# Kernel optimization log

Measured on AMD Instinct MI355X. Metric: run time of the kernel, lower is better.

Reference implementation:

```python
import jax, jax.numpy as jnp
import numpy as np


def setup_inputs() -> dict:
    key = jax.random.key(0)
    k1, k2 = jax.random.split(key)
    B, N, M = 8, 8192, 8192
    pred = jax.random.normal(k1, (B, N, 3), dtype=jnp.float32)
    gt = jax.random.normal(k2, (B, M, 3), dtype=jnp.float32)
    return {"pred": pred, "gt": gt}


def _chamfer(pred, gt):
    # pred: [B,N,3], gt: [B,M,3]
    # squared pairwise distances: ||p||^2 + ||q||^2 - 2 p.q  -> [B,N,M]
    p_sq = jnp.sum(pred * pred, axis=-1)           # [B,N]
    q_sq = jnp.sum(gt * gt, axis=-1)               # [B,M]
    cross = jnp.einsum('bnd,bmd->bnm', pred, gt)   # [B,N,M]
    dist = p_sq[:, :, None] + q_sq[:, None, :] - 2.0 * cross
    dist = jnp.maximum(dist, 0.0)  # numerical floor, distances are non-negative
    # kaolin chamfer_distance: mean over points of nearest-neighbor sq-dist, both sides
    p2q = jnp.mean(jnp.min(dist, axis=2), axis=1)  # [B]
    q2p = jnp.mean(jnp.min(dist, axis=1), axis=1)  # [B]
    chamfer = p2q + q2p                            # [B] (w1 = w2 = 1)
    return jnp.mean(chamfer)                       # scalar, torch.mean over batch


def reference(pred, gt):
    return _chamfer(pred, gt)
```

## Files before the change

### kernel.cpp

```cpp
#include <hip/hip_runtime.h>


typedef short bf16x8 __attribute__((ext_vector_type(8)));
typedef float f32x16 __attribute__((ext_vector_type(16)));

#define B_SZ   8
#define NPTS   8192
#define TOTAL  (B_SZ * NPTS)
#define BLOCK  256
#define QB     256
#define SLICE  1024
#define NSTAGE (NPTS / SLICE)
#define TILES  (SLICE / 32)

__device__ __forceinline__ unsigned short bf16rn(float f, float* rem) {
    unsigned u = __float_as_uint(f);
    unsigned h = (u + 0x8000u) & 0xFFFF0000u;
    *rem = f - __uint_as_float(h);
    return (unsigned short)(h >> 16);
}

__global__ __launch_bounds__(BLOCK) void chamfer_prep_mfma(
    const float* __restrict__ gt, const float* __restrict__ pred,
    uint4* __restrict__ TgA, uint4* __restrict__ TgB, float* __restrict__ Wg,
    uint4* __restrict__ TpA, uint4* __restrict__ TpB, float* __restrict__ Wp)
{
    int i = blockIdx.x * BLOCK + threadIdx.x;
    const float* src = blockIdx.y ? pred : gt;
    uint4* TA = blockIdx.y ? TpA : TgA;
    uint4* TB = blockIdx.y ? TpB : TgB;
    float* W  = blockIdx.y ? Wp  : Wg;

    float x = src[3 * (size_t)i + 0];
    float y = src[3 * (size_t)i + 1];
    float z = src[3 * (size_t)i + 2];
    float w = fmaf(x, x, fmaf(y, y, z * z));
    W[i] = w;

    float ux = -2.f * x, uy = -2.f * y, uz = -2.f * z;
    float rx, ry, rz, dx, dy, dz, rw1, rw2, rw3;
    unsigned short uhx = bf16rn(ux, &rx), uhy = bf16rn(uy, &ry), uhz = bf16rn(uz, &rz);
    unsigned short ulx = bf16rn(rx, &dx), uly = bf16rn(ry, &dy), ulz = bf16rn(rz, &dz);
    unsigned short wh = bf16rn(w, &rw1), wm = bf16rn(rw1, &rw2), wl = bf16rn(rw2, &rw3);
    union { unsigned short s[16]; uint4 v[2]; } A;
    A.s[0] = uhx; A.s[1] = uhy; A.s[2]  = uhz;
    A.s[3] = uhx; A.s[4] = uhy; A.s[5]  = uhz;
    A.s[6] = ulx; A.s[7] = uly; A.s[8]  = ulz;
    A.s[9] = ulx; A.s[10] = uly; A.s[11] = ulz;
    A.s[12] = wh; A.s[13] = wm; A.s[14] = wl; A.s[15] = 0;
    TA[2 * (size_t)i]     = A.v[0];
    TA[2 * (size_t)i + 1] = A.v[1];

    float sx, sy, sz, ex, ey, ez;
    unsigned short qhx = bf16rn(x, &sx), qhy = bf16rn(y, &sy), qhz = bf16rn(z, &sz);
    unsigned short qlx = bf16rn(sx, &ex), qly = bf16rn(sy, &ey), qlz = bf16rn(sz, &ez);
    union { unsigned short s[16]; uint4 v[2]; } Bb;
    Bb.s[0] = qhx; Bb.s[1] = qhy; Bb.s[2]  = qhz;
    Bb.s[3] = qlx; Bb.s[4] = qly; Bb.s[5]  = qlz;
    Bb.s[6] = qhx; Bb.s[7] = qhy; Bb.s[8]  = qhz;
    Bb.s[9] = qlx; Bb.s[10] = qly; Bb.s[11] = qlz;
    Bb.s[12] = 0x3F80; Bb.s[13] = 0x3F80; Bb.s[14] = 0x3F80; Bb.s[15] = 0;
    TB[2 * (size_t)i]     = Bb.v[0];
    TB[2 * (size_t)i + 1] = Bb.v[1];
}

__device__ __forceinline__ float minred(f32x16 d, float m) {
    float r0 = fminf(fminf(d[0], d[1]), d[2]);
    float r1 = fminf(fminf(d[3], d[4]), d[5]);
    float r2 = fminf(fminf(d[6], d[7]), d[8]);
    float r3 = fminf(fminf(d[9], d[10]), d[11]);
    float r4 = fminf(fminf(d[12], d[13]), d[14]);
    float s0 = fminf(fminf(r0, r1), r2);
    float s1 = fminf(fminf(r3, r4), d[15]);
    return fminf(fminf(m, s0), s1);
}

__global__ __launch_bounds__(BLOCK, 2) void chamfer_nn_fused(
    const uint4* __restrict__ TgA, const uint4* __restrict__ TpB,
    const float* __restrict__ Wp,
    const uint4* __restrict__ TpA, const uint4* __restrict__ TgB,
    const float* __restrict__ Wg,
    float* __restrict__ out)
{
    __shared__ uint4 tileU[SLICE * 2];
    __shared__ float psum[4];
    char* tileC = (char*)tileU;

    const int qb = blockIdx.x, b = blockIdx.y, dir = blockIdx.z;
    const int t = threadIdx.x, lane = t & 63, wid = t >> 6;
    const int col = lane & 31, hi = lane >> 5;

    const uint4* TA = dir ? TpA : TgA;
    const uint4* TB = dir ? TgB : TpB;
    const float* WQ = dir ? Wg  : Wp;

    const int qblk = qb * QB + wid * 64;
    const char* TBc = (const char*)(TB + ((size_t)b * NPTS + qblk) * 2);
    bf16x8 bq0 = *(const bf16x8*)(TBc + (size_t)col * 32 + hi * 16);
    bf16x8 bq1 = *(const bf16x8*)(TBc + (size_t)(col + 32) * 32 + hi * 16);

    f32x16 zacc;
#pragma unroll
    for (int j = 0; j < 16; ++j) zacc[j] = 0.f;
    float m0 = 3.0e38f, m1 = 3.0e38f;
    const int abase = (col * 32 + hi * 16) ^ (((col >> 2) & 7) << 4);

    for (int st = 0; st < NSTAGE; ++st) {
        const uint4* srcA = TA + ((size_t)b * NPTS + (size_t)st * SLICE) * 2;
#pragma unroll
        for (int it = 0; it < (SLICE * 2) / BLOCK; ++it) {
            int g = t + it * BLOCK;
            uint4 v = srcA[g];
            int tl = g >> 1, gh = g & 1;
            int off = (tl * 32 + gh * 16) ^ (((tl >> 2) & 7) << 4);
            *(uint4*)(tileC + off) = v;
        }
        __syncthreads();

#pragma unroll 2
        for (int tt = 0; tt < TILES; ++tt) {
            bf16x8 a = *(const bf16x8*)(tileC + abase + tt * 1024);
            f32x16 d0 = __builtin_amdgcn_mfma_f32_32x32x16_bf16(a, bq0, zacc, 0, 0, 0);
            m0 = minred(d0, m0);
            f32x16 d1 = __builtin_amdgcn_mfma_f32_32x32x16_bf16(a, bq1, zacc, 0, 0, 0);
            m1 = minred(d1, m1);
        }
        __syncthreads();
    }

    m0 = fminf(m0, __shfl_xor(m0, 32));
    m1 = fminf(m1, __shfl_xor(m1, 32));
    float wq = WQ[(size_t)b * NPTS + qb * QB + t];
    float d = fmaxf((lane < 32 ? m0 : m1) + wq, 0.0f);
    float s = d;
#pragma unroll
    for (int o = 1; o < 64; o <<= 1) s += __shfl_xor(s, o);
    if (lane == 0) psum[wid] = s;
    __syncthreads();
    if (t == 0) {
        float tot = (psum[0] + psum[1]) + (psum[2] + psum[3]);
        atomicAdd(out, tot * (1.0f / (float)TOTAL));
    }
}

extern "C" void kernel_launch(void* const* d_in, const int* in_sizes, int n_in,
                              void* d_out, int out_size, void* d_ws, size_t ws_size,
                              hipStream_t stream) {
    const float* pred = (const float*)d_in[0];
    const float* gt   = (const float*)d_in[1];
    float* out = (float*)d_out;

    char* ws = (char*)d_ws;
    uint4* TgA = (uint4*)(ws);
    uint4* TpA = (uint4*)(ws + (size_t)TOTAL * 32);
    uint4* TgB = (uint4*)(ws + (size_t)TOTAL * 64);
    uint4* TpB = (uint4*)(ws + (size_t)TOTAL * 96);
    float* Wg  = (float*)(ws + (size_t)TOTAL * 128);
    float* Wp  = (float*)(ws + (size_t)TOTAL * 128 + (size_t)TOTAL * 4);

    hipMemsetAsync(out, 0, sizeof(float), stream);

    chamfer_prep_mfma<<<dim3(TOTAL / BLOCK, 2), BLOCK, 0, stream>>>(
        gt, pred, TgA, TgB, Wg, TpA, TpB, Wp);

    chamfer_nn_fused<<<dim3(NPTS / QB, B_SZ, 2), BLOCK, 0, stream>>>(
        TgA, TpB, Wp, TpA, TgB, Wg, out);
}
```

Measured before the change: 99.64 us.

## Double-buffer slices with async global-to-LDS loads and defer min reduction

Replaces the register-staged global→LDS copy with direct global_load_lds transfers into a double-buffered shared tile. The next slice is prefetched while the current one is computed, and one barrier per stage is dropped. The source lane index is pre-swizzled to match the existing XOR bank layout. The per-tile scalar min reduction is replaced by elementwise min into two 16-wide accumulator vectors, reduced once at the end, and the next A fragment is loaded from LDS one tile ahead. This doubles LDS use to 64KB per block, which may limit occupancy, and adds 32 registers of min accumulators.

```diff
diff --git a/kernel.cpp b/kernel.cpp
--- a/kernel.cpp
+++ b/kernel.cpp
@@ -64,15 +64,27 @@
     TB[2 * (size_t)i + 1] = Bb.v[1];
 }
 
-__device__ __forceinline__ float minred(f32x16 d, float m) {
-    float r0 = fminf(fminf(d[0], d[1]), d[2]);
-    float r1 = fminf(fminf(d[3], d[4]), d[5]);
-    float r2 = fminf(fminf(d[6], d[7]), d[8]);
-    float r3 = fminf(fminf(d[9], d[10]), d[11]);
-    float r4 = fminf(fminf(d[12], d[13]), d[14]);
+__device__ __forceinline__ void gload_lds16(const void* g, void* l) {
+    __builtin_amdgcn_global_load_lds(
+        (const __attribute__((address_space(1))) unsigned int*)g,
+        (__attribute__((address_space(3))) unsigned int*)l, 16, 0, 0);
+}
+
+__device__ __forceinline__ f32x16 min16(f32x16 m, f32x16 d) {
+#pragma unroll
+    for (int j = 0; j < 16; ++j) m[j] = fminf(m[j], d[j]);
+    return m;
+}
+
+__device__ __forceinline__ float mintree(f32x16 m) {
+    float r0 = fminf(fminf(m[0], m[1]), m[2]);
+    float r1 = fminf(fminf(m[3], m[4]), m[5]);
+    float r2 = fminf(fminf(m[6], m[7]), m[8]);
+    float r3 = fminf(fminf(m[9], m[10]), m[11]);
+    float r4 = fminf(fminf(m[12], m[13]), m[14]);
     float s0 = fminf(fminf(r0, r1), r2);
-    float s1 = fminf(fminf(r3, r4), d[15]);
-    return fminf(fminf(m, s0), s1);
+    float s1 = fminf(fminf(r3, r4), m[15]);
+    return fminf(s0, s1);
 }
 
 __global__ __launch_bounds__(BLOCK, 2) void chamfer_nn_fused(
@@ -82,7 +94,7 @@
     const float* __restrict__ Wg,
     float* __restrict__ out)
 {
-    __shared__ uint4 tileU[SLICE * 2];
+    __shared__ uint4 tileU[2 * SLICE * 2];
     __shared__ float psum[4];
     char* tileC = (char*)tileU;
 
@@ -102,32 +114,51 @@
     f32x16 zacc;
 #pragma unroll
     for (int j = 0; j < 16; ++j) zacc[j] = 0.f;
-    float m0 = 3.0e38f, m1 = 3.0e38f;
+    f32x16 macc0 = zacc + 3.0e38f;
+    f32x16 macc1 = macc0;
     const int abase = (col * 32 + hi * 16) ^ (((col >> 2) & 7) << 4);
 
+    const uint4* TAb = TA + (size_t)b * NPTS * 2;
+    const int swzlane = lane ^ (lane >> 3);
+    const uint4* gsrc0 = TAb + wid * 512 + swzlane;
+    char* ldst0 = tileC + wid * 8192;
+
+#pragma unroll
+    for (int it = 0; it < 8; ++it)
+        gload_lds16(gsrc0 + it * 64, ldst0 + it * 1024);
+    __syncthreads();
+
     for (int st = 0; st < NSTAGE; ++st) {
-        const uint4* srcA = TA + ((size_t)b * NPTS + (size_t)st * SLICE) * 2;
+        const int cur = (st & 1) << 15;
+        if (st + 1 < NSTAGE) {
+            const uint4* gs = gsrc0 + (size_t)(st + 1) * (SLICE * 2);
+            char* ld = ldst0 + (cur ^ 32768);
 #pragma unroll
-        for (int it = 0; it < (SLICE * 2) / BLOCK; ++it) {
-            int g = t + it * BLOCK;
-            uint4 v = srcA[g];
-            int tl = g >> 1, gh = g & 1;
-            int off = (tl * 32 + gh * 16) ^ (((tl >> 2) & 7) << 4);
-            *(uint4*)(tileC + off) = v;
+            for (int it = 0; it < 8; ++it)
+                gload_lds16(gs + it * 64, ld + it * 1024);
         }
-        __syncthreads();
 
+        const char* tb = tileC + cur + abase;
+        bf16x8 a_cur = *(const bf16x8*)(tb);
 #pragma unroll 2
-        for (int tt = 0; tt < TILES; ++tt) {
-            bf16x8 a = *(const bf16x8*)(tileC + abase + tt * 1024);
-            f32x16 d0 = __builtin_amdgcn_mfma_f32_32x32x16_bf16(a, bq0, zacc, 0, 0, 0);
-            m0 = minred(d0, m0);
-            f32x16 d1 = __builtin_amdgcn_mfma_f32_32x32x16_bf16(a, bq1, zacc, 0, 0, 0);
-            m1 = minred(d1, m1);
+        for (int tt = 0; tt < TILES - 1; ++tt) {
+            bf16x8 a_nxt = *(const bf16x8*)(tb + (tt + 1) * 1024);
+            f32x16 d0 = __builtin_amdgcn_mfma_f32_32x32x16_bf16(a_cur, bq0, zacc, 0, 0, 0);
+            f32x16 d1 = __builtin_amdgcn_mfma_f32_32x32x16_bf16(a_cur, bq1, zacc, 0, 0, 0);
+            macc0 = min16(macc0, d0);
+            macc1 = min16(macc1, d1);
+            a_cur = a_nxt;
         }
+        f32x16 d0 = __builtin_amdgcn_mfma_f32_32x32x16_bf16(a_cur, bq0, zacc, 0, 0, 0);
+        f32x16 d1 = __builtin_amdgcn_mfma_f32_32x32x16_bf16(a_cur, bq1, zacc, 0, 0, 0);
+        macc0 = min16(macc0, d0);
+        macc1 = min16(macc1, d1);
+
         __syncthreads();
     }
 
+    float m0 = mintree(macc0);
+    float m1 = mintree(macc1);
     m0 = fminf(m0, __shfl_xor(m0, 32));
     m1 = fminf(m1, __shfl_xor(m1, 32));
     float wq = WQ[(size_t)b * NPTS + qb * QB + t];
```

After: 97.69 us. About the same (-2.0%).
